# Performance work log

Measured on AMD Instinct MI355X. Metric: run time of the kernel, lower is better.

## Reference

```python
import jax, jax.numpy as jnp
import numpy as np

P = 16          # num_points (knots per piecewise-linear function)
LO, HI = -1.0, 1.0  # uniform knot grid range
EPS = 1e-6


def apl(x, v):
    """Adaptive piecewise-linear layer on a uniform grid.
    x: (N, I), v: (I, P, O) learnable knot values. out[n,o] = sum_i interp_i(x[n,i])."""
    I, Pk, O = v.shape
    t = (jnp.clip(x, LO, HI) - LO) / (HI - LO) * (Pk - 1)   # (N, I) in [0, P-1]
    idx = jnp.clip(jnp.floor(t), 0, Pk - 2).astype(jnp.int32)
    frac = t - idx
    ar = jnp.arange(Pk)
    # sparse interpolation weights (N, I, P): two nonzeros per (n, i)
    w = (jnp.where(ar == idx[..., None], (1.0 - frac)[..., None], 0.0)
         + jnp.where(ar == idx[..., None] + 1, frac[..., None], 0.0))
    return jnp.einsum('nip,ipo->no', w, v)


def max_abs_normalize(h):
    B, T, D = h.shape
    hn = h.reshape(B * T, D)
    hn = hn / (jnp.max(jnp.abs(hn), axis=1, keepdims=True) + EPS)
    return hn.reshape(B, T, D)


def mingru_layer(x, h0, vz, vh):
    """x: (B,T,Din), h0: (B,D). Returns normalized hidden states (B,T,D)."""
    B, T, _ = x.shape
    xf = x.reshape(B * T, -1)
    h_bar = apl(xf, vh).reshape(B, T, -1)
    z = jax.nn.sigmoid(apl(xf, vz)).reshape(B, T, -1)
    a = 1.0 - z
    b = z * h_bar
    # unstable closed-form recurrence: h[t] = A[t] * (h0 + cumsum(b/A))
    A = jnp.cumprod(a, axis=1)
    S = jnp.cumsum(b / A, axis=1)
    h = A * (h0[:, None, :] + S)
    return max_abs_normalize(h)


def setup_inputs() -> dict:
    key = jax.random.key(0)
    ks = jax.random.split(key, 8)
    B, T, Din, D, Dout = 8, 2048, 64, 64, 64
    Z_OFF = -6.0 / Din  # bias z-layer output to ~-6 so sigmoid(z) is small -> cumprod stays finite
    x = jax.random.normal(ks[0], (B, T, Din), dtype=jnp.float32)
    def vz(k, I, O):
        return 0.05 * jax.random.normal(k, (I, P, O), dtype=jnp.float32) + Z_OFF
    def vh(k, I, O):
        return 0.5 * jax.random.normal(k, (I, P, O), dtype=jnp.float32)
    return {
        'x': x,
        'vz0': vz(ks[1], Din, D), 'vh0': vh(ks[2], Din, D),
        'vz1': vz(ks[3], D, D),   'vh1': vh(ks[4], D, D),
        'vz2': vz(ks[5], D, D),   'vh2': vh(ks[6], D, D),
        'vout': 0.5 * jax.random.normal(ks[7], (D, P, Dout), dtype=jnp.float32),
    }


def reference(x, vz0, vh0, vz1, vh1, vz2, vh2, vout):
    B, T, _ = x.shape
    D = vh0.shape[-1]
    h0 = jnp.zeros((B, D), dtype=x.dtype)
    cur = mingru_layer(x, h0, vz0, vh0)
    cur = mingru_layer(cur, h0, vz1, vh1)
    cur = mingru_layer(cur, h0, vz2, vh2)
    out = apl(cur.reshape(B * T, -1), vout).reshape(B, T, -1)
    return out
```

## Files before the change

### kernel.cpp

```cpp
#include <hip/hip_runtime.h>


#define WPB 8
#define NC 64
#define CL 32

__device__ __forceinline__ unsigned int pack_bf16(float f) {
    unsigned int u = __float_as_uint(f);
    return (u + 0x7fffu + ((u >> 16) & 1u)) >> 16;
}

__global__ __launch_bounds__(256) void prep_dual_kernel(
    const float* __restrict__ vz, const float* __restrict__ vh,
    float4* __restrict__ tab)
{
    int idx = blockIdx.x * blockDim.x + threadIdx.x;
    if (idx >= 64 * 15 * 64) return;
    int o = idx & 63;
    int p = (idx >> 6) % 15;
    int i = idx / (15 * 64);
    int base = (i * 16 + p) * 64 + o;
    float z0 = vz[base], z1 = vz[base + 64];
    float h0 = vh[base], h1 = vh[base + 64];
    tab[idx] = make_float4(z0, z1 - z0, h0, h1 - h0);
}

__global__ __launch_bounds__(256) void prep_out_kernel(
    const float* __restrict__ v, unsigned int* __restrict__ tab)
{
    int idx = blockIdx.x * blockDim.x + threadIdx.x;
    if (idx >= 64 * 15 * 64) return;
    int o = idx & 63;
    int p = (idx >> 6) % 15;
    int i = idx / (15 * 64);
    int base = (i * 16 + p) * 64 + o;
    float v0 = v[base], v1 = v[base + 64];
    tab[idx] = pack_bf16(v0) | (pack_bf16(v1 - v0) << 16);
}

__global__ __launch_bounds__(512) void apl_dual_kernel(
    const float* __restrict__ in, const float4* __restrict__ tab,
    float2* __restrict__ zh, int N)
{
    const int lane = threadIdx.x & 63;
    const int n = blockIdx.x * WPB + (threadIdx.x >> 6);
    if (n >= N) return;

    float xv = in[(size_t)n * 64 + lane];
    float tv = fminf(fmaxf(xv, -1.f), 1.f) * 7.5f + 7.5f;
    int iv = (int)tv; iv = iv > 14 ? 14 : iv;
    float frv = tv - (float)iv;
    int offv = lane * 15360 + (iv << 10);

    const char* tb = (const char*)tab + lane * 16;
    float accz0 = 0.f, acch0 = 0.f, accz1 = 0.f, acch1 = 0.f;
#pragma unroll
    for (int i0 = 0; i0 < 64; i0 += 4) {
        int of0 = __shfl(offv, i0 + 0, 64);
        int of1 = __shfl(offv, i0 + 1, 64);
        int of2 = __shfl(offv, i0 + 2, 64);
        int of3 = __shfl(offv, i0 + 3, 64);
        float fr0 = __shfl(frv, i0 + 0, 64);
        float fr1 = __shfl(frv, i0 + 1, 64);
        float fr2 = __shfl(frv, i0 + 2, 64);
        float fr3 = __shfl(frv, i0 + 3, 64);
        float4 e0 = *(const float4*)(tb + of0);
        float4 e1 = *(const float4*)(tb + of1);
        float4 e2 = *(const float4*)(tb + of2);
        float4 e3 = *(const float4*)(tb + of3);
        accz0 += fmaf(fr0, e0.y, e0.x);
        acch0 += fmaf(fr0, e0.w, e0.z);
        accz1 += fmaf(fr1, e1.y, e1.x);
        acch1 += fmaf(fr1, e1.w, e1.z);
        accz0 += fmaf(fr2, e2.y, e2.x);
        acch0 += fmaf(fr2, e2.w, e2.z);
        accz1 += fmaf(fr3, e3.y, e3.x);
        acch1 += fmaf(fr3, e3.w, e3.z);
    }
    float accz = accz0 + accz1, acch = acch0 + acch1;
    float z = 1.f / (1.f + expf(-accz));
    zh[(size_t)n * 64 + lane] = make_float2(z, acch);
}

__global__ __launch_bounds__(512) void apl_out_kernel(
    const float* __restrict__ in, const unsigned int* __restrict__ tab,
    float* __restrict__ out, int N)
{
    const int lane = threadIdx.x & 63;
    const int n = blockIdx.x * WPB + (threadIdx.x >> 6);
    if (n >= N) return;

    float xv = in[(size_t)n * 64 + lane];
    float tv = fminf(fmaxf(xv, -1.f), 1.f) * 7.5f + 7.5f;
    int iv = (int)tv; iv = iv > 14 ? 14 : iv;
    float frv = tv - (float)iv;
    int offv = lane * 3840 + (iv << 8);

    const char* tb = (const char*)tab + lane * 4;
    float acc0 = 0.f, acc1 = 0.f;
#pragma unroll
    for (int i0 = 0; i0 < 64; i0 += 8) {
        int of[8]; float fr[8]; unsigned int e[8];
#pragma unroll
        for (int j = 0; j < 8; ++j) of[j] = __shfl(offv, i0 + j, 64);
#pragma unroll
        for (int j = 0; j < 8; ++j) fr[j] = __shfl(frv, i0 + j, 64);
#pragma unroll
        for (int j = 0; j < 8; ++j) e[j] = *(const unsigned int*)(tb + of[j]);
#pragma unroll
        for (int j = 0; j < 8; j += 2) {
            acc0 += fmaf(fr[j], __uint_as_float(e[j] & 0xffff0000u),
                         __uint_as_float(e[j] << 16));
            acc1 += fmaf(fr[j + 1], __uint_as_float(e[j + 1] & 0xffff0000u),
                         __uint_as_float(e[j + 1] << 16));
        }
    }
    out[(size_t)n * 64 + lane] = acc0 + acc1;
}

__global__ __launch_bounds__(256) void scan_pass1_kernel(
    const float2* __restrict__ zh, float2* __restrict__ chunkAB, int T)
{
    int lane = threadIdx.x & 63;
    int wid = blockIdx.x * (blockDim.x >> 6) + (threadIdx.x >> 6);
    int b = wid / NC, c = wid % NC;
    const float2* p = zh + ((size_t)b * T + (size_t)c * CL) * 64 + lane;

    float A = 1.f, Bc = 0.f;
    for (int k0 = 0; k0 < CL; k0 += 8) {
        float2 v[8];
#pragma unroll
        for (int k = 0; k < 8; ++k) v[k] = p[(size_t)(k0 + k) * 64];
#pragma unroll
        for (int k = 0; k < 8; ++k) {
            float a = 1.f - v[k].x;
            float bb = v[k].x * v[k].y;
            A *= a;
            Bc = fmaf(a, Bc, bb);
        }
    }
    chunkAB[(size_t)wid * 64 + lane] = make_float2(A, Bc);
}

__global__ __launch_bounds__(64) void scan_fixup_kernel(
    const float2* __restrict__ chunkAB, float* __restrict__ hinit)
{
    int b = blockIdx.x;
    int d = threadIdx.x;
    const float2* p = chunkAB + (size_t)b * NC * 64 + d;
    float* o = hinit + (size_t)b * NC * 64 + d;

    float h = 0.f;
    for (int c0 = 0; c0 < NC; c0 += 8) {
        float2 ab[8];
#pragma unroll
        for (int k = 0; k < 8; ++k) ab[k] = p[(size_t)(c0 + k) * 64];
#pragma unroll
        for (int k = 0; k < 8; ++k) {
            o[(size_t)(c0 + k) * 64] = h;
            h = fmaf(ab[k].x, h, ab[k].y);
        }
    }
}

__global__ __launch_bounds__(256) void scan_pass2_kernel(
    const float2* __restrict__ zh, const float* __restrict__ hinit,
    float* __restrict__ out, int T)
{
    int lane = threadIdx.x & 63;
    int wid = blockIdx.x * (blockDim.x >> 6) + (threadIdx.x >> 6);
    int b = wid / NC, c = wid % NC;
    const float2* p = zh + ((size_t)b * T + (size_t)c * CL) * 64 + lane;
    float* o = out + ((size_t)b * T + (size_t)c * CL) * 64 + lane;

    float h = hinit[(size_t)wid * 64 + lane];
    for (int k0 = 0; k0 < CL; k0 += 8) {
        float2 v[8];
        float hs[8];
#pragma unroll
        for (int k = 0; k < 8; ++k) v[k] = p[(size_t)(k0 + k) * 64];
#pragma unroll
        for (int k = 0; k < 8; ++k) {
            h = fmaf(v[k].x, v[k].y - h, h);
            hs[k] = h;
        }
#pragma unroll
        for (int k = 0; k < 8; ++k) {
            float m = fabsf(hs[k]);
            m = fmaxf(m, __shfl_xor(m, 32, 64));
            m = fmaxf(m, __shfl_xor(m, 16, 64));
            m = fmaxf(m, __shfl_xor(m, 8, 64));
            m = fmaxf(m, __shfl_xor(m, 4, 64));
            m = fmaxf(m, __shfl_xor(m, 2, 64));
            m = fmaxf(m, __shfl_xor(m, 1, 64));
            o[(size_t)(k0 + k) * 64] = hs[k] / (m + 1e-6f);
        }
    }
}

extern "C" void kernel_launch(void* const* d_in, const int* in_sizes, int n_in,
                              void* d_out, int out_size, void* d_ws, size_t ws_size,
                              hipStream_t stream) {
    const float* x    = (const float*)d_in[0];
    const float* vz0  = (const float*)d_in[1];
    const float* vh0  = (const float*)d_in[2];
    const float* vz1  = (const float*)d_in[3];
    const float* vh1  = (const float*)d_in[4];
    const float* vz2  = (const float*)d_in[5];
    const float* vh2  = (const float*)d_in[6];
    const float* vout = (const float*)d_in[7];

    const int N = in_sizes[0] / 64;
    const int T = NC * CL;
    const int B = N / T;

    char* ws = (char*)d_ws;
    const size_t TAB_ELEMS = (size_t)64 * 15 * 64;
    float2* zh      = (float2*)ws;
    float*  cur     = (float*)(ws + 8388608);
    float4* tab0    = (float4*)(ws + 12582912);
    float4* tab1    = (float4*)(ws + 13565952);
    float4* tab2    = (float4*)(ws + 14548992);
    unsigned int* tab_out = (unsigned int*)(ws + 15532032);
    float2* chunkAB = (float2*)(ws + 16023552);
    float*  hinit   = (float*)(ws + 16285696);

    dim3 pblk(256), pgrd((TAB_ELEMS + 255) / 256);
    prep_dual_kernel<<<pgrd, pblk, 0, stream>>>(vz0, vh0, tab0);
    prep_dual_kernel<<<pgrd, pblk, 0, stream>>>(vz1, vh1, tab1);
    prep_dual_kernel<<<pgrd, pblk, 0, stream>>>(vz2, vh2, tab2);
    prep_out_kernel<<<pgrd, pblk, 0, stream>>>(vout, tab_out);

    dim3 ablk(64 * WPB), agrd((N + WPB - 1) / WPB);
    dim3 sblk(256), sgrd(B * NC / 4);

    const float4* tabs[3] = {tab0, tab1, tab2};
    const float* layer_in = x;
    for (int l = 0; l < 3; ++l) {
        apl_dual_kernel<<<agrd, ablk, 0, stream>>>(layer_in, tabs[l], zh, N);
        scan_pass1_kernel<<<sgrd, sblk, 0, stream>>>(zh, chunkAB, T);
        scan_fixup_kernel<<<B, 64, 0, stream>>>(chunkAB, hinit);
        scan_pass2_kernel<<<sgrd, sblk, 0, stream>>>(zh, hinit, cur, T);
        layer_in = cur;
    }
    apl_out_kernel<<<agrd, ablk, 0, stream>>>(cur, tab_out, (float*)d_out, N);
}
```

Before: 186.1 us.

## Stage APL tables in LDS per input feature and batch 64 rows per block

Replaces the per-row gather APL kernel with one where each 512-thread block handles 64 rows, streams each input feature's 15x64 table slice into double-buffered shared memory, and reuses it across 8 rows per wave, using readlane broadcasts for index and fraction. This aims to cut the repeated random global/L2 gathers of the table, which now load once per block. The output table also switches from bf16 to fp16 packing, which changes precision and range. The new kernel assumes N is a multiple of 64 and adds a barrier per input feature.

```diff
diff --git a/kernel.cpp b/kernel.cpp
--- a/kernel.cpp
+++ b/kernel.cpp
@@ -1,13 +1,20 @@
 #include <hip/hip_runtime.h>
+#include <hip/hip_fp16.h>
 
 
 #define WPB 8
 #define NC 64
 #define CL 32
 
-__device__ __forceinline__ unsigned int pack_bf16(float f) {
-    unsigned int u = __float_as_uint(f);
-    return (u + 0x7fffu + ((u >> 16) & 1u)) >> 16;
+__device__ __forceinline__ unsigned int pack_f16(float lo, float hi) {
+    return (unsigned int)__half_as_ushort(__float2half(lo))
+         | ((unsigned int)__half_as_ushort(__float2half(hi)) << 16);
+}
+__device__ __forceinline__ float unpack_f16_lo(unsigned int u) {
+    return __half2float(__ushort_as_half((unsigned short)(u & 0xffffu)));
+}
+__device__ __forceinline__ float unpack_f16_hi(unsigned int u) {
+    return __half2float(__ushort_as_half((unsigned short)(u >> 16)));
 }
 
 __global__ __launch_bounds__(256) void prep_dual_kernel(
@@ -35,51 +42,74 @@
     int i = idx / (15 * 64);
     int base = (i * 16 + p) * 64 + o;
     float v0 = v[base], v1 = v[base + 64];
-    tab[idx] = pack_bf16(v0) | (pack_bf16(v1 - v0) << 16);
-}
-
-__global__ __launch_bounds__(512) void apl_dual_kernel(
+    tab[idx] = pack_f16(v0, v1 - v0);
+}
+
+__global__ __launch_bounds__(512) void apl_dual_lds_kernel(
     const float* __restrict__ in, const float4* __restrict__ tab,
-    float2* __restrict__ zh, int N)
-{
-    const int lane = threadIdx.x & 63;
-    const int n = blockIdx.x * WPB + (threadIdx.x >> 6);
-    if (n >= N) return;
-
-    float xv = in[(size_t)n * 64 + lane];
-    float tv = fminf(fmaxf(xv, -1.f), 1.f) * 7.5f + 7.5f;
-    int iv = (int)tv; iv = iv > 14 ? 14 : iv;
-    float frv = tv - (float)iv;
-    int offv = lane * 15360 + (iv << 10);
-
-    const char* tb = (const char*)tab + lane * 16;
-    float accz0 = 0.f, acch0 = 0.f, accz1 = 0.f, acch1 = 0.f;
-#pragma unroll
-    for (int i0 = 0; i0 < 64; i0 += 4) {
-        int of0 = __shfl(offv, i0 + 0, 64);
-        int of1 = __shfl(offv, i0 + 1, 64);
-        int of2 = __shfl(offv, i0 + 2, 64);
-        int of3 = __shfl(offv, i0 + 3, 64);
-        float fr0 = __shfl(frv, i0 + 0, 64);
-        float fr1 = __shfl(frv, i0 + 1, 64);
-        float fr2 = __shfl(frv, i0 + 2, 64);
-        float fr3 = __shfl(frv, i0 + 3, 64);
-        float4 e0 = *(const float4*)(tb + of0);
-        float4 e1 = *(const float4*)(tb + of1);
-        float4 e2 = *(const float4*)(tb + of2);
-        float4 e3 = *(const float4*)(tb + of3);
-        accz0 += fmaf(fr0, e0.y, e0.x);
-        acch0 += fmaf(fr0, e0.w, e0.z);
-        accz1 += fmaf(fr1, e1.y, e1.x);
-        acch1 += fmaf(fr1, e1.w, e1.z);
-        accz0 += fmaf(fr2, e2.y, e2.x);
-        acch0 += fmaf(fr2, e2.w, e2.z);
-        accz1 += fmaf(fr3, e3.y, e3.x);
-        acch1 += fmaf(fr3, e3.w, e3.z);
-    }
-    float accz = accz0 + accz1, acch = acch0 + acch1;
-    float z = 1.f / (1.f + expf(-accz));
-    zh[(size_t)n * 64 + lane] = make_float2(z, acch);
+    float2* __restrict__ zh)
+{
+    __shared__ float slc[2][4][960];
+
+    const int tid = threadIdx.x;
+    const int lane = tid & 63;
+    const int w = tid >> 6;
+    const size_t nb = (size_t)blockIdx.x * 64 + (size_t)w * 8;
+
+    int   iv8[8];
+    float fr8[8];
+#pragma unroll
+    for (int s = 0; s < 8; ++s) {
+        float xv = in[(nb + s) * 64 + lane];
+        float tv = fminf(fmaxf(xv, -1.f), 1.f) * 7.5f + 7.5f;
+        int iv = (int)tv; iv = iv > 14 ? 14 : iv;
+        iv8[s] = iv;
+        fr8[s] = tv - (float)iv;
+    }
+
+    float accz[8], acch[8];
+#pragma unroll
+    for (int s = 0; s < 8; ++s) { accz[s] = 0.f; acch[s] = 0.f; }
+
+    float4 e0 = tab[tid];
+    float4 e1 = make_float4(0.f, 0.f, 0.f, 0.f);
+    if (tid < 448) e1 = tab[tid + 512];
+
+#pragma unroll 2
+    for (int i = 0; i < 64; ++i) {
+        const int buf = i & 1;
+        slc[buf][0][tid] = e0.x; slc[buf][1][tid] = e0.y;
+        slc[buf][2][tid] = e0.z; slc[buf][3][tid] = e0.w;
+        if (tid < 448) {
+            slc[buf][0][tid + 512] = e1.x; slc[buf][1][tid + 512] = e1.y;
+            slc[buf][2][tid + 512] = e1.z; slc[buf][3][tid + 512] = e1.w;
+        }
+        if (i < 63) {
+            const float4* src = tab + (size_t)(i + 1) * 960;
+            e0 = src[tid];
+            if (tid < 448) e1 = src[tid + 512];
+        }
+        __syncthreads();
+#pragma unroll
+        for (int s = 0; s < 8; ++s) {
+            int idx  = __builtin_amdgcn_readlane(iv8[s], i);
+            float fr = __int_as_float(
+                __builtin_amdgcn_readlane(__float_as_int(fr8[s]), i));
+            int r = idx * 64 + lane;
+            float z0 = slc[buf][0][r];
+            float dz = slc[buf][1][r];
+            float h0 = slc[buf][2][r];
+            float dh = slc[buf][3][r];
+            accz[s] += fmaf(fr, dz, z0);
+            acch[s] += fmaf(fr, dh, h0);
+        }
+    }
+
+#pragma unroll
+    for (int s = 0; s < 8; ++s) {
+        float z = 1.f / (1.f + expf(-accz[s]));
+        zh[(nb + s) * 64 + lane] = make_float2(z, acch[s]);
+    }
 }
 
 __global__ __launch_bounds__(512) void apl_out_kernel(
@@ -109,10 +139,8 @@
         for (int j = 0; j < 8; ++j) e[j] = *(const unsigned int*)(tb + of[j]);
 #pragma unroll
         for (int j = 0; j < 8; j += 2) {
-            acc0 += fmaf(fr[j], __uint_as_float(e[j] & 0xffff0000u),
-                         __uint_as_float(e[j] << 16));
-            acc1 += fmaf(fr[j + 1], __uint_as_float(e[j + 1] & 0xffff0000u),
-                         __uint_as_float(e[j + 1] << 16));
+            acc0 += fmaf(fr[j], unpack_f16_hi(e[j]), unpack_f16_lo(e[j]));
+            acc1 += fmaf(fr[j + 1], unpack_f16_hi(e[j + 1]), unpack_f16_lo(e[j + 1]));
         }
     }
     out[(size_t)n * 64 + lane] = acc0 + acc1;
@@ -231,13 +259,14 @@
     prep_dual_kernel<<<pgrd, pblk, 0, stream>>>(vz2, vh2, tab2);
     prep_out_kernel<<<pgrd, pblk, 0, stream>>>(vout, tab_out);
 
+    dim3 lblk(512), lgrd(N / 64);
     dim3 ablk(64 * WPB), agrd((N + WPB - 1) / WPB);
     dim3 sblk(256), sgrd(B * NC / 4);
 
     const float4* tabs[3] = {tab0, tab1, tab2};
     const float* layer_in = x;
     for (int l = 0; l < 3; ++l) {
-        apl_dual_kernel<<<agrd, ablk, 0, stream>>>(layer_in, tabs[l], zh, N);
+        apl_dual_lds_kernel<<<lgrd, lblk, 0, stream>>>(layer_in, tabs[l], zh);
         scan_pass1_kernel<<<sgrd, sblk, 0, stream>>>(zh, chunkAB, T);
         scan_fixup_kernel<<<B, 64, 0, stream>>>(chunkAB, hinit);
         scan_pass2_kernel<<<sgrd, sblk, 0, stream>>>(zh, hinit, cur, T);
```

After: 204.1 us. 9.7% more time.
